# Optimization experiments

Hardware: AMD Instinct MI355X
Metric: run time of the kernel (lower is better)

The kernel has to match this reference:

```python
import jax, jax.numpy as jnp
import numpy as np

E = 800000   # num edges
N = 50000    # num atoms
C = 128      # in_channels
RBF = 20     # rbf_dim
T = 1        # num_target


def setup_inputs() -> dict:
    key = jax.random.key(0)
    ks = jax.random.split(key, 12)
    return {
        "x_scalar": jax.random.normal(ks[0], (E, C), dtype=jnp.float32),
        "rbf": jax.random.normal(ks[1], (E, RBF), dtype=jnp.float32),
        "envelop_para": jax.random.uniform(ks[2], (E, 1), dtype=jnp.float32),
        "edge_index_0": jax.random.randint(ks[3], (E,), 0, N),
        "num_atoms": N,
        # learned parameters (biases initialized to zero per reset_parameters)
        "W_rbf": jax.random.normal(ks[4], (C, RBF), dtype=jnp.float32) * 0.05,
        "b_rbf": jnp.zeros((C,), dtype=jnp.float32),
        "W1": jax.random.normal(ks[5], (C, C), dtype=jnp.float32) * 0.05,
        "b1": jnp.zeros((C,), dtype=jnp.float32),
        "W2": jax.random.normal(ks[6], (C, C), dtype=jnp.float32) * 0.05,
        "b2": jnp.zeros((C,), dtype=jnp.float32),
        "W3": jax.random.normal(ks[7], (T, C), dtype=jnp.float32) * 0.05,
        "b3": jnp.zeros((T,), dtype=jnp.float32),
    }


def reference(x_scalar, rbf, envelop_para, edge_index_0, num_atoms,
              W_rbf, b_rbf, W1, b1, W2, b2, W3, b3):
    # per-edge filter: Linear(rbf) * envelope, then modulate node features
    rbf_filter = (rbf @ W_rbf.T + b_rbf) * envelop_para  # [E, C]
    msg = rbf_filter * x_scalar                           # [E, C]
    # scatter_add over destination atoms
    out = jax.ops.segment_sum(msg, edge_index_0, num_segments=num_atoms)  # [N, C]
    # small MLP head: Linear+SiLU, Linear+SiLU, Linear -> num_target
    out = jax.nn.silu(out @ W1.T + b1)
    out = jax.nn.silu(out @ W2.T + b2)
    out = out @ W3.T + b3                                 # [N, T]
    return out
```

## Files before the change

### kernel.cpp

```cpp
#include <hip/hip_runtime.h>
#include <hip/hip_bf16.h>

#define C 128
#define RBFD 20
#define NATOMS 50000
#define SCAN_CHUNK 1024
#define SLAB 256
#define SS 32

__global__ __launch_bounds__(256) void setup_kernel(
    const float* __restrict__ W1, const float* __restrict__ W2,
    float* __restrict__ W1T, float* __restrict__ W2T,
    int* __restrict__ count, float4* __restrict__ acc4,
    int n, int acc_quads)
{
    const int t = blockIdx.x * blockDim.x + threadIdx.x;
    const int stride = gridDim.x * blockDim.x;
    if (t < C * C) {
        int k = t / C;
        int c = t % C;
        W1T[t] = W1[c * C + k];
        W2T[t] = W2[c * C + k];
    }
    for (int i = t; i < n; i += stride) count[i] = 0;
    const float4 z = make_float4(0.f, 0.f, 0.f, 0.f);
    for (int i = t; i < acc_quads; i += stride) acc4[i] = z;
}

__global__ __launch_bounds__(256) void histogram_kernel(
    const int* __restrict__ idx, int* __restrict__ count, int E)
{
    int e = blockIdx.x * blockDim.x + threadIdx.x;
    if (e < E) atomicAdd(&count[idx[e]], 1);
}

__global__ __launch_bounds__(256) void scan_partials_kernel(
    const int* __restrict__ count, int* __restrict__ partial, int n)
{
    __shared__ int sm[256];
    const int start = blockIdx.x * SCAN_CHUNK;
    int s = 0;
    for (int i = threadIdx.x; i < SCAN_CHUNK; i += 256) {
        int g = start + i;
        if (g < n) s += count[g];
    }
    sm[threadIdx.x] = s;
    __syncthreads();
    for (int off = 128; off > 0; off >>= 1) {
        if (threadIdx.x < off) sm[threadIdx.x] += sm[threadIdx.x + off];
        __syncthreads();
    }
    if (threadIdx.x == 0) partial[blockIdx.x] = sm[0];
}

__global__ void scan_chunkbase_kernel(int* __restrict__ partial,
                                      int* __restrict__ base,
                                      int nchunks, int n)
{
    if (threadIdx.x == 0 && blockIdx.x == 0) {
        int run = 0;
        for (int k = 0; k < nchunks; ++k) {
            int t = partial[k];
            partial[k] = run;
            run += t;
        }
        base[n] = run;
    }
}

__global__ __launch_bounds__(1024) void scan_apply_kernel(
    const int* __restrict__ count, const int* __restrict__ chunk_base,
    int* __restrict__ base, int* __restrict__ cursor, int n)
{
    __shared__ int sm[SCAN_CHUNK];
    const int t = threadIdx.x;
    const int i = blockIdx.x * SCAN_CHUNK + t;
    int v = (i < n) ? count[i] : 0;
    sm[t] = v;
    __syncthreads();
    for (int off = 1; off < SCAN_CHUNK; off <<= 1) {
        int tmp = (t >= off) ? sm[t - off] : 0;
        __syncthreads();
        sm[t] += tmp;
        __syncthreads();
    }
    if (i < n) {
        int excl = sm[t] - v + chunk_base[blockIdx.x];
        base[i] = excl;
        cursor[i] = excl;
    }
}

__global__ __launch_bounds__(256) void fill_perm_kernel(
    const int* __restrict__ idx, int* __restrict__ cursor,
    int* __restrict__ perm, int* __restrict__ own, int E)
{
    int e = blockIdx.x * blockDim.x + threadIdx.x;
    if (e < E) {
        int a = idx[e];
        int pos = atomicAdd(&cursor[a], 1);
        perm[pos] = e;
        own[pos] = a;
    }
}

__global__ __launch_bounds__(128, 3) void gather_kernel(
    const float* __restrict__ x,
    const float* __restrict__ rbf,
    const float* __restrict__ env,
    const int*   __restrict__ perm,
    const int*   __restrict__ own,
    const float* __restrict__ Wrbf,
    const float* __restrict__ brbf,
    float* __restrict__ acc)
{
    __shared__ int   e_s[SLAB];
    __shared__ float env_s[SLAB];
    __shared__ int   own_s[SLAB];

    const int tid = threadIdx.x;
    const int p0  = blockIdx.x * SLAB;

    for (int i = tid; i < SLAB; i += 128) {
        const int e = perm[p0 + i];
        e_s[i]   = e;
        env_s[i] = env[e];
        own_s[i] = own[p0 + i];
    }

    float w[RBFD];
#pragma unroll
    for (int r = 0; r < RBFD; ++r) w[r] = Wrbf[tid * RBFD + r];
    const float bias = brbf[tid];

    __syncthreads();

    const int first_own = own_s[0];
    int   cur = first_own;
    float sum = 0.0f;

#define FLUSH()                                                            \
    do {                                                                   \
        if (cur == first_own) unsafeAtomicAdd(&acc[(size_t)cur * C + tid], sum); \
        else                  acc[(size_t)cur * C + tid] = sum;            \
    } while (0)

    for (int s = 0; s < SLAB; s += SS) {
        float xr[SS];
#pragma unroll
        for (int i = 0; i < SS; ++i)
            xr[i] = x[(size_t)e_s[s + i] * C + tid];

#pragma unroll
        for (int j = 0; j < SS; j += 2) {
            const int e0 = e_s[s + j];
            const int e1 = e_s[s + j + 1];
            const float4* q0 = reinterpret_cast<const float4*>(rbf + (size_t)e0 * RBFD);
            const float4* q1 = reinterpret_cast<const float4*>(rbf + (size_t)e1 * RBFD);
            float4 A0 = q0[0], A1 = q0[1], A2 = q0[2], A3 = q0[3], A4 = q0[4];
            float4 B0 = q1[0], B1 = q1[1], B2 = q1[2], B3 = q1[3], B4 = q1[4];

            float f0 = bias, f1 = bias;
            f0 = fmaf(A0.x,w[0],f0);  f0 = fmaf(A0.y,w[1],f0);
            f0 = fmaf(A0.z,w[2],f0);  f0 = fmaf(A0.w,w[3],f0);
            f0 = fmaf(A1.x,w[4],f0);  f0 = fmaf(A1.y,w[5],f0);
            f0 = fmaf(A1.z,w[6],f0);  f0 = fmaf(A1.w,w[7],f0);
            f0 = fmaf(A2.x,w[8],f0);  f0 = fmaf(A2.y,w[9],f0);
            f0 = fmaf(A2.z,w[10],f0); f0 = fmaf(A2.w,w[11],f0);
            f0 = fmaf(A3.x,w[12],f0); f0 = fmaf(A3.y,w[13],f0);
            f0 = fmaf(A3.z,w[14],f0); f0 = fmaf(A3.w,w[15],f0);
            f0 = fmaf(A4.x,w[16],f0); f0 = fmaf(A4.y,w[17],f0);
            f0 = fmaf(A4.z,w[18],f0); f0 = fmaf(A4.w,w[19],f0);

            f1 = fmaf(B0.x,w[0],f1);  f1 = fmaf(B0.y,w[1],f1);
            f1 = fmaf(B0.z,w[2],f1);  f1 = fmaf(B0.w,w[3],f1);
            f1 = fmaf(B1.x,w[4],f1);  f1 = fmaf(B1.y,w[5],f1);
            f1 = fmaf(B1.z,w[6],f1);  f1 = fmaf(B1.w,w[7],f1);
            f1 = fmaf(B2.x,w[8],f1);  f1 = fmaf(B2.y,w[9],f1);
            f1 = fmaf(B2.z,w[10],f1); f1 = fmaf(B2.w,w[11],f1);
            f1 = fmaf(B3.x,w[12],f1); f1 = fmaf(B3.y,w[13],f1);
            f1 = fmaf(B3.z,w[14],f1); f1 = fmaf(B3.w,w[15],f1);
            f1 = fmaf(B4.x,w[16],f1); f1 = fmaf(B4.y,w[17],f1);
            f1 = fmaf(B4.z,w[18],f1); f1 = fmaf(B4.w,w[19],f1);

            const float v0 = f0 * env_s[s + j]     * xr[j];
            const float v1 = f1 * env_s[s + j + 1] * xr[j + 1];

            const int o0 = own_s[s + j];
            const int o1 = own_s[s + j + 1];
            if (o0 != cur) { FLUSH(); sum = 0.0f; cur = o0; }
            sum += v0;
            if (o1 != cur) { FLUSH(); sum = 0.0f; cur = o1; }
            sum += v1;
        }
    }
    unsafeAtomicAdd(&acc[(size_t)cur * C + tid], sum);
#undef FLUSH
}

__device__ __forceinline__ float silu_f(float v) {
    return v * (1.0f / (1.0f + __expf(-v)));
}

__global__ __launch_bounds__(256) void mlp_head_kernel(
    const float* __restrict__ acc,
    const float* __restrict__ W1T,
    const float* __restrict__ b1,
    const float* __restrict__ W2T,
    const float* __restrict__ b2,
    const float* __restrict__ W3,
    const float* __restrict__ b3,
    float* __restrict__ out,
    int natoms)
{
    __shared__ float As[C][C + 1];

    const int tid = threadIdx.x;
    const int a0  = blockIdx.x * C;
    const int tc  = tid & 15;
    const int ta  = tid >> 4;
    const int abase = ta * 8;
    const int cbase = tc * 8;

    {
        const int sub = tid >> 7;
        const int k   = tid & 127;
        for (int pair = 0; pair < 64; ++pair) {
            const int al = pair * 2 + sub;
            const int a  = a0 + al;
            float v = (a < natoms) ? acc[(size_t)a * C + k] : 0.0f;
            As[k][al] = v;
        }
    }
    __syncthreads();

    float r[8][8];

#pragma unroll
    for (int i = 0; i < 8; ++i)
#pragma unroll
        for (int j = 0; j < 8; ++j) r[i][j] = 0.0f;

#pragma unroll 2
    for (int k = 0; k < C; ++k) {
        float4 bq0 = *reinterpret_cast<const float4*>(W1T + k * C + cbase);
        float4 bq1 = *reinterpret_cast<const float4*>(W1T + k * C + cbase + 4);
        float bv[8] = {bq0.x, bq0.y, bq0.z, bq0.w, bq1.x, bq1.y, bq1.z, bq1.w};
        float av[8];
#pragma unroll
        for (int i = 0; i < 8; ++i) av[i] = As[k][abase + i];
#pragma unroll
        for (int i = 0; i < 8; ++i)
#pragma unroll
            for (int j = 0; j < 8; ++j) r[i][j] = fmaf(av[i], bv[j], r[i][j]);
    }

    __syncthreads();
    {
        float bb[8];
#pragma unroll
        for (int j = 0; j < 8; ++j) bb[j] = b1[cbase + j];
#pragma unroll
        for (int i = 0; i < 8; ++i)
#pragma unroll
            for (int j = 0; j < 8; ++j)
                As[cbase + j][abase + i] = silu_f(r[i][j] + bb[j]);
    }
    __syncthreads();

#pragma unroll
    for (int i = 0; i < 8; ++i)
#pragma unroll
        for (int j = 0; j < 8; ++j) r[i][j] = 0.0f;

#pragma unroll 2
    for (int k = 0; k < C; ++k) {
        float4 bq0 = *reinterpret_cast<const float4*>(W2T + k * C + cbase);
        float4 bq1 = *reinterpret_cast<const float4*>(W2T + k * C + cbase + 4);
        float bv[8] = {bq0.x, bq0.y, bq0.z, bq0.w, bq1.x, bq1.y, bq1.z, bq1.w};
        float av[8];
#pragma unroll
        for (int i = 0; i < 8; ++i) av[i] = As[k][abase + i];
#pragma unroll
        for (int i = 0; i < 8; ++i)
#pragma unroll
            for (int j = 0; j < 8; ++j) r[i][j] = fmaf(av[i], bv[j], r[i][j]);
    }

    __syncthreads();

    {
        float bb[8], w3v[8];
#pragma unroll
        for (int j = 0; j < 8; ++j) bb[j] = b2[cbase + j];
        float4 wq0 = *reinterpret_cast<const float4*>(W3 + cbase);
        float4 wq1 = *reinterpret_cast<const float4*>(W3 + cbase + 4);
        w3v[0]=wq0.x; w3v[1]=wq0.y; w3v[2]=wq0.z; w3v[3]=wq0.w;
        w3v[4]=wq1.x; w3v[5]=wq1.y; w3v[6]=wq1.z; w3v[7]=wq1.w;

#pragma unroll
        for (int i = 0; i < 8; ++i) {
            float p = 0.0f;
#pragma unroll
            for (int j = 0; j < 8; ++j)
                p = fmaf(silu_f(r[i][j] + bb[j]), w3v[j], p);
            As[abase + i][tc] = p;
        }
    }
    __syncthreads();

    if (tid < C) {
        const int a = a0 + tid;
        if (a < natoms) {
            float s = 0.0f;
#pragma unroll
            for (int t = 0; t < 16; ++t) s += As[tid][t];
            out[a] = s + b3[0];
        }
    }
}

extern "C" void kernel_launch(void* const* d_in, const int* in_sizes, int n_in,
                              void* d_out, int out_size, void* d_ws, size_t ws_size,
                              hipStream_t stream) {
    const float* x      = (const float*)d_in[0];
    const float* rbf    = (const float*)d_in[1];
    const float* env    = (const float*)d_in[2];
    const int*   idx    = (const int*)  d_in[3];
    const float* Wrbf   = (const float*)d_in[5];
    const float* brbf   = (const float*)d_in[6];
    const float* W1     = (const float*)d_in[7];
    const float* b1     = (const float*)d_in[8];
    const float* W2     = (const float*)d_in[9];
    const float* b2     = (const float*)d_in[10];
    const float* W3     = (const float*)d_in[11];
    const float* b3     = (const float*)d_in[12];
    float*       out    = (float*)d_out;

    const int E = in_sizes[0] / C;
    const int N = NATOMS;
    const int nchunks = (N + SCAN_CHUNK - 1) / SCAN_CHUNK;

    float* acc     = (float*)d_ws;
    float* W1T     = acc + (size_t)N * C;
    float* W2T     = W1T + C * C;
    int*   count   = (int*)(W2T + C * C);
    int*   base    = count + N;
    int*   cursor  = base + (N + 1);
    int*   partial = cursor + N;
    int*   perm    = partial + 64;
    int*   own     = perm + E;

    setup_kernel<<<2048, 256, 0, stream>>>(W1, W2, W1T, W2T, count,
                                           (float4*)acc, N, (N * C) / 4);

    histogram_kernel<<<(E + 255) / 256, 256, 0, stream>>>(idx, count, E);
    scan_partials_kernel<<<nchunks, 256, 0, stream>>>(count, partial, N);
    scan_chunkbase_kernel<<<1, 64, 0, stream>>>(partial, base, nchunks, N);
    scan_apply_kernel<<<nchunks, SCAN_CHUNK, 0, stream>>>(count, partial, base, cursor, N);
    fill_perm_kernel<<<(E + 255) / 256, 256, 0, stream>>>(idx, cursor, perm, own, E);

    gather_kernel<<<E / SLAB, 128, 0, stream>>>(x, rbf, env, perm, own,
                                                Wrbf, brbf, acc);

    const int tiles = (N + C - 1) / C;
    mlp_head_kernel<<<tiles, 256, 0, stream>>>(acc, W1T, b1, W2T, b2, W3, b3, out, N);
}
```

Measured before the change: 407.5 us.

## Software-pipeline rbf loads in gather kernel and halve slab size

Prefetches the next pair of edges' rbf rows before computing the current pair's 20-wide dot products, with sched_barriers forcing the loads to issue early and overlap with the FMAs. SLAB drops from 256 to 128, so each block does one load per thread in the prologue and the grid has twice as many blocks. The outer loop is no longer unrolled and the occupancy hint drops from 3 to 2 blocks per CU. The prefetch raises register pressure, the smaller slab adds more boundary atomics, and the sched_barriers may stop the compiler from scheduling well on its own.

Result: faster. 365.9 us (-10.2%).

```diff
diff --git a/kernel.cpp b/kernel.cpp
--- a/kernel.cpp
+++ b/kernel.cpp
@@ -5,7 +5,7 @@
 #define RBFD 20
 #define NATOMS 50000
 #define SCAN_CHUNK 1024
-#define SLAB 256
+#define SLAB 128
 #define SS 32
 
 __global__ __launch_bounds__(256) void setup_kernel(
@@ -104,7 +104,32 @@
     }
 }
 
-__global__ __launch_bounds__(128, 3) void gather_kernel(
+struct R5 { float4 a, b, c, d, e; };
+
+__device__ __forceinline__ R5 load_rbf5(const float* __restrict__ rbf, int eidx) {
+    const float4* q = reinterpret_cast<const float4*>(rbf + (size_t)eidx * RBFD);
+    R5 r;
+    r.a = q[0]; r.b = q[1]; r.c = q[2]; r.d = q[3]; r.e = q[4];
+    return r;
+}
+
+__device__ __forceinline__ float dot20(const R5& p, const float* __restrict__ w,
+                                       float bias) {
+    float f = bias;
+    f = fmaf(p.a.x, w[0],  f); f = fmaf(p.a.y, w[1],  f);
+    f = fmaf(p.a.z, w[2],  f); f = fmaf(p.a.w, w[3],  f);
+    f = fmaf(p.b.x, w[4],  f); f = fmaf(p.b.y, w[5],  f);
+    f = fmaf(p.b.z, w[6],  f); f = fmaf(p.b.w, w[7],  f);
+    f = fmaf(p.c.x, w[8],  f); f = fmaf(p.c.y, w[9],  f);
+    f = fmaf(p.c.z, w[10], f); f = fmaf(p.c.w, w[11], f);
+    f = fmaf(p.d.x, w[12], f); f = fmaf(p.d.y, w[13], f);
+    f = fmaf(p.d.z, w[14], f); f = fmaf(p.d.w, w[15], f);
+    f = fmaf(p.e.x, w[16], f); f = fmaf(p.e.y, w[17], f);
+    f = fmaf(p.e.z, w[18], f); f = fmaf(p.e.w, w[19], f);
+    return f;
+}
+
+__global__ __launch_bounds__(128, 2) void gather_kernel(
     const float* __restrict__ x,
     const float* __restrict__ rbf,
     const float* __restrict__ env,
@@ -121,11 +146,11 @@
     const int tid = threadIdx.x;
     const int p0  = blockIdx.x * SLAB;
 
-    for (int i = tid; i < SLAB; i += 128) {
-        const int e = perm[p0 + i];
-        e_s[i]   = e;
-        env_s[i] = env[e];
-        own_s[i] = own[p0 + i];
+    {
+        const int e = perm[p0 + tid];
+        e_s[tid]   = e;
+        env_s[tid] = env[e];
+        own_s[tid] = own[p0 + tid];
     }
 
     float w[RBFD];
@@ -139,49 +164,35 @@
     int   cur = first_own;
     float sum = 0.0f;
 
-#define FLUSH()                                                            \
-    do {                                                                   \
+#define FLUSH()                                                                \
+    do {                                                                       \
         if (cur == first_own) unsafeAtomicAdd(&acc[(size_t)cur * C + tid], sum); \
-        else                  acc[(size_t)cur * C + tid] = sum;            \
+        else                  acc[(size_t)cur * C + tid] = sum;                \
     } while (0)
 
+#pragma unroll 1
     for (int s = 0; s < SLAB; s += SS) {
         float xr[SS];
 #pragma unroll
         for (int i = 0; i < SS; ++i)
             xr[i] = x[(size_t)e_s[s + i] * C + tid];
+        __builtin_amdgcn_sched_barrier(0);
+
+        R5 Pa = load_rbf5(rbf, e_s[s + 0]);
+        R5 Pb = load_rbf5(rbf, e_s[s + 1]);
+        __builtin_amdgcn_sched_barrier(0);
 
 #pragma unroll
         for (int j = 0; j < SS; j += 2) {
-            const int e0 = e_s[s + j];
-            const int e1 = e_s[s + j + 1];
-            const float4* q0 = reinterpret_cast<const float4*>(rbf + (size_t)e0 * RBFD);
-            const float4* q1 = reinterpret_cast<const float4*>(rbf + (size_t)e1 * RBFD);
-            float4 A0 = q0[0], A1 = q0[1], A2 = q0[2], A3 = q0[3], A4 = q0[4];
-            float4 B0 = q1[0], B1 = q1[1], B2 = q1[2], B3 = q1[3], B4 = q1[4];
-
-            float f0 = bias, f1 = bias;
-            f0 = fmaf(A0.x,w[0],f0);  f0 = fmaf(A0.y,w[1],f0);
-            f0 = fmaf(A0.z,w[2],f0);  f0 = fmaf(A0.w,w[3],f0);
-            f0 = fmaf(A1.x,w[4],f0);  f0 = fmaf(A1.y,w[5],f0);
-            f0 = fmaf(A1.z,w[6],f0);  f0 = fmaf(A1.w,w[7],f0);
-            f0 = fmaf(A2.x,w[8],f0);  f0 = fmaf(A2.y,w[9],f0);
-            f0 = fmaf(A2.z,w[10],f0); f0 = fmaf(A2.w,w[11],f0);
-            f0 = fmaf(A3.x,w[12],f0); f0 = fmaf(A3.y,w[13],f0);
-            f0 = fmaf(A3.z,w[14],f0); f0 = fmaf(A3.w,w[15],f0);
-            f0 = fmaf(A4.x,w[16],f0); f0 = fmaf(A4.y,w[17],f0);
-            f0 = fmaf(A4.z,w[18],f0); f0 = fmaf(A4.w,w[19],f0);
-
-            f1 = fmaf(B0.x,w[0],f1);  f1 = fmaf(B0.y,w[1],f1);
-            f1 = fmaf(B0.z,w[2],f1);  f1 = fmaf(B0.w,w[3],f1);
-            f1 = fmaf(B1.x,w[4],f1);  f1 = fmaf(B1.y,w[5],f1);
-            f1 = fmaf(B1.z,w[6],f1);  f1 = fmaf(B1.w,w[7],f1);
-            f1 = fmaf(B2.x,w[8],f1);  f1 = fmaf(B2.y,w[9],f1);
-            f1 = fmaf(B2.z,w[10],f1); f1 = fmaf(B2.w,w[11],f1);
-            f1 = fmaf(B3.x,w[12],f1); f1 = fmaf(B3.y,w[13],f1);
-            f1 = fmaf(B3.z,w[14],f1); f1 = fmaf(B3.w,w[15],f1);
-            f1 = fmaf(B4.x,w[16],f1); f1 = fmaf(B4.y,w[17],f1);
-            f1 = fmaf(B4.z,w[18],f1); f1 = fmaf(B4.w,w[19],f1);
+            R5 Na, Nb;
+            if (j + 2 < SS) {
+                Na = load_rbf5(rbf, e_s[s + j + 2]);
+                Nb = load_rbf5(rbf, e_s[s + j + 3]);
+            }
+            __builtin_amdgcn_sched_barrier(0);
+
+            const float f0 = dot20(Pa, w, bias);
+            const float f1 = dot20(Pb, w, bias);
 
             const float v0 = f0 * env_s[s + j]     * xr[j];
             const float v1 = f1 * env_s[s + j + 1] * xr[j + 1];
@@ -192,6 +203,8 @@
             sum += v0;
             if (o1 != cur) { FLUSH(); sum = 0.0f; cur = o1; }
             sum += v1;
+
+            if (j + 2 < SS) { Pa = Na; Pb = Nb; }
         }
     }
     unsafeAtomicAdd(&acc[(size_t)cur * C + tid], sum);
```
